# Performance work log

Measured on AMD Instinct MI355X. Metric: run time of the kernel, lower is better.

Reference implementation:

```python
import jax, jax.numpy as jnp
import numpy as np

EPS = 2e-5
NCG = 51  # int(64 / 1.25)

def _conv1d(x, w, d):
    # x: [B,C,L], w: [Co,Ci,K]; dilated 1D conv, SAME padding
    return jax.lax.conv_general_dilated(x, w, window_strides=(1,), padding='SAME',
                                        rhs_dilation=(d,), dimension_numbers=('NCH', 'OIH', 'NCH'))

def _lift(x, w, n_h=9):
    # GConvRdG: lift R1 -> R1xR+; scale h=2^s realized as kernel dilation, 1/h normalization
    return jnp.stack([_conv1d(x, w, 2 ** s) / (2.0 ** s) for s in range(n_h)], axis=2)

def _gg(x, w):
    # GConvGG on [B,C,H,L]; w: [Co,Ci,Nk,K]; h_crop: H_out = H - Nk + 1.
    # Output scale s mixes input scales s..s+Nk-1, each with spatial dilation 2^(s+i).
    Nk, H = w.shape[2], x.shape[2]
    outs = []
    for s in range(H - Nk + 1):
        acc = None
        for i in range(Nk):
            d = 2 ** (s + i)
            t = _conv1d(x[:, :, s + i, :], w[:, :, i, :], d) / float(d)
            acc = t if acc is None else acc + t
        outs.append(acc)
    return jnp.stack(outs, axis=2)

def _bn(x, g, b):
    # training-mode BatchNorm2d over [B,C,H,L], per-channel stats
    m = jnp.mean(x, axis=(0, 2, 3), keepdims=True)
    v = jnp.var(x, axis=(0, 2, 3), keepdims=True)
    return (x - m) * jax.lax.rsqrt(v + EPS) * g[None, :, None, None] + b[None, :, None, None]

def _pool4(x):
    # max_pooling_R1: kernel 4 stride 4 over spatial axis
    B, C, H, L = x.shape
    return jnp.max(x.reshape(B, C, H, L // 4, 4), axis=-1)

def _forward(x, w1, w2, w3, w4, w5, w6, w7, w8, w9, w10, w11,
             g1, b1, g2, b2, g3, b3, g4, b4, g5, b5, g6, b6, g7, b7, g8, b8, g9, b9, g10, b10):
    r = jax.nn.relu
    out = _lift(x, w1)                      # [B,51,9,L]
    out = _pool4(out)
    out = r(_bn(out, g1, b1))
    out = _pool4(out)
    out = r(_bn(_gg(out, w2), g2, b2))      # H 9->7
    out = r(_bn(_gg(out, w3), g3, b3))
    out = _pool4(out)
    out = r(_bn(_gg(out, w4), g4, b4))      # 7->5
    out = r(_bn(_gg(out, w5), g5, b5))
    out = _pool4(out)
    out = r(_bn(_gg(out, w6), g6, b6))      # 5->3
    out = r(_bn(_gg(out, w7), g7, b7))
    out = r(_bn(_gg(out, w8), g8, b8))
    out = _pool4(out)
    out = r(_bn(_gg(out, w9), g9, b9))      # 3->1
    out = r(_bn(_gg(out, w10), g10, b10))
    out = jnp.mean(out, axis=-1, keepdims=True)   # global mean over space -> [B,408,1,1]
    out = _gg(out, w11)                     # 1x1 classifier -> [B,10,1,1]
    out = jnp.max(out, axis=-2)             # max over h axis -> [B,10,1]
    return out.reshape(out.shape[0], 10)

def setup_inputs():
    key = jax.random.key(0)
    ks = jax.random.split(key, 16)
    c = NCG
    def w(k, shape):
        fan_in = float(np.prod(shape[1:]))
        return jax.random.normal(k, shape, jnp.float32) * fan_in ** -0.5
    inp = {
        'x': jax.random.normal(ks[0], (8, 1, 32768), jnp.float32),
        'w1': w(ks[1], (c, 1, 79)),
        'w2': w(ks[2], (c, c, 3, 3)),
        'w3': w(ks[3], (c, c, 1, 3)),
        'w4': w(ks[4], (2 * c, c, 3, 3)),
        'w5': w(ks[5], (2 * c, 2 * c, 1, 3)),
        'w6': w(ks[6], (4 * c, 2 * c, 3, 3)),
        'w7': w(ks[7], (4 * c, 4 * c, 1, 3)),
        'w8': w(ks[8], (4 * c, 4 * c, 1, 3)),
        'w9': w(ks[9], (8 * c, 4 * c, 3, 3)),
        'w10': w(ks[10], (8 * c, 8 * c, 1, 3)),
        'w11': w(ks[11], (10, 8 * c, 1, 1)),
    }
    widths = [c, c, c, 2 * c, 2 * c, 4 * c, 4 * c, 4 * c, 8 * c, 8 * c]
    for i, cw in enumerate(widths, 1):
        inp['g%d' % i] = jnp.ones((cw,), jnp.float32)
        inp['b%d' % i] = jnp.zeros((cw,), jnp.float32)
    return inp

def reference(x, w1, w2, w3, w4, w5, w6, w7, w8, w9, w10, w11,
              g1, b1, g2, b2, g3, b3, g4, b4, g5, b5, g6, b6, g7, b7, g8, b8, g9, b9, g10, b10):
    return _forward(x, w1, w2, w3, w4, w5, w6, w7, w8, w9, w10, w11,
                    g1, b1, g2, b2, g3, b3, g4, b4, g5, b5, g6, b6, g7, b7, g8, b8, g9, b9, g10, b10)
```

## Files before the change

### kernel.cpp

```cpp
#include <hip/hip_runtime.h>
#include <hip/hip_bf16.h>

#define EPSBN 2e-5f

typedef __attribute__((ext_vector_type(8))) short short8v;
typedef __attribute__((ext_vector_type(4))) float f32x4;

__device__ inline unsigned short f2bf(float f) {
  unsigned u = __float_as_uint(f);
  unsigned r = (u + 0x7FFFu + ((u >> 16) & 1u)) >> 16;
  return (unsigned short)r;
}
__device__ inline float bf2f(unsigned short h) {
  return __uint_as_float(((unsigned)h) << 16);
}

template <int CTRL>
__device__ inline float dpp_radd(float v) {
  int r = __builtin_amdgcn_update_dpp(0, __float_as_int(v), CTRL, 0xf, 0xf,
                                      true);
  return v + __int_as_float(r);
}

constexpr int XPADL = 9984;
constexpr int XPADR = 14336;
constexpr int PROW = XPADL + 32768 + XPADR;

__global__ __launch_bounds__(256) void pad_pair_kernel(
    const float* __restrict__ x, unsigned* __restrict__ xpH,
    unsigned* __restrict__ xpL) {
  const int i = blockIdx.x * 256 + threadIdx.x;
  if (i >= PROW) return;
  const int sb = blockIdx.y;
  const int s = sb >> 3;
  const int b = sb & 7;
  const int d = 1 << s;
  const int pos0 = i - XPADL;
  const int pos1 = pos0 + d;
  float v0 = (pos0 >= 0 && pos0 < 32768) ? x[b * 32768 + pos0] : 0.f;
  float v1 = (pos1 >= 0 && pos1 < 32768) ? x[b * 32768 + pos1] : 0.f;
  unsigned u0 = __float_as_uint(v0);
  unsigned h0 = u0 >> 16;
  unsigned lo0 =
      __float_as_uint(v0 - __uint_as_float(u0 & 0xffff0000u)) >> 16;
  unsigned u1 = __float_as_uint(v1);
  unsigned h1 = u1 >> 16;
  unsigned lo1 =
      __float_as_uint(v1 - __uint_as_float(u1 & 0xffff0000u)) >> 16;
  size_t o = (size_t)sb * PROW + i;
  xpH[o] = h0 | (h1 << 16);
  xpL[o] = lo0 | (lo1 << 16);
}

__global__ __launch_bounds__(256) void pack_w1_kernel(
    const float* __restrict__ W, short* __restrict__ A) {
  int idx = blockIdx.x * 256 + threadIdx.x;
  if (idx >= 9 * 64 * 96) return;
  int s = idx / (64 * 96);
  int rem = idx - s * 64 * 96;
  int co = rem / 96;
  int k = rem - co * 96;
  float v = 0.f;
  if (co < 51 && k < 79)
    v = W[co * 79 + k] * __uint_as_float((unsigned)(127 - s) << 23);
  unsigned short hi = f2bf(v);
  unsigned short lo = f2bf(v - bf2f(hi));
  A[(size_t)s * 2 * 64 * 96 + co * 96 + k] = (short)hi;
  A[(size_t)s * 2 * 64 * 96 + 64 * 96 + co * 96 + k] = (short)lo;
}

__global__ __launch_bounds__(256) void lift_mfma_kernel(
    const unsigned* __restrict__ xpH, const unsigned* __restrict__ xpL,
    const short* __restrict__ Apk1, float* __restrict__ y1,
    float* __restrict__ part1) {
  constexpr int P = 104;
  const int bid = blockIdx.x;
  const int lc = (bid & 7) * 64 + (bid >> 3);
  const int s = blockIdx.y;
  const int b = blockIdx.z;
  const int d = 1 << s;
  const int l0 = lc * 64;
  const int tid = threadIdx.x;
  const int lane = tid & 63;
  const int quad = lane >> 4;
  const int n0 = lane & 15;
  const int wv = tid >> 6;
  const int coBase = wv * 16;

  __shared__ __align__(16) short Bh[64 * P];
  __shared__ __align__(16) short Bl[64 * P];
  float* sC = (float*)Bh;

  const int nB = tid & 63;
  const int rowW = ((nB & 3) << 4) | (nB >> 2);
  const int swzW = (nB & 3) << 3;
  const int ogu = __builtin_amdgcn_readfirstlane(tid >> 6);
  const unsigned* xqH = xpH + (size_t)(s * 8 + b) * PROW + XPADL + l0;
  const unsigned* xqL = xpL + (size_t)(s * 8 + b) * PROW + XPADL + l0;

#pragma unroll
  for (int r = 0; r < 3; ++r) {
    const int kb = (ogu + 4 * r) * 8;
    const int base = (kb - 39) * d;
    uint4 ph, pl;
    ph.x = xqH[base + nB];
    ph.y = xqH[base + 2 * d + nB];
    ph.z = xqH[base + 4 * d + nB];
    ph.w = xqH[base + 6 * d + nB];
    pl.x = xqL[base + nB];
    pl.y = xqL[base + 2 * d + nB];
    pl.z = xqL[base + 4 * d + nB];
    pl.w = xqL[base + 6 * d + nB];
    *(uint4*)(Bh + rowW * P + (kb ^ swzW)) = ph;
    *(uint4*)(Bl + rowW * P + (kb ^ swzW)) = pl;
  }

  const short* ApkS = Apk1 + (size_t)s * 2 * 64 * 96;
  const short* arowH = ApkS + (coBase + n0) * 96;
  const short* arowL = arowH + 64 * 96;

  __syncthreads();

  f32x4 acc[4];
#pragma unroll
  for (int t = 0; t < 4; ++t) acc[t] = (f32x4){0.f, 0.f, 0.f, 0.f};

#pragma unroll
  for (int ks = 0; ks < 3; ++ks) {
    short8v ah = *(const short8v*)(arowH + ks * 32 + quad * 8);
    short8v al = *(const short8v*)(arowL + ks * 32 + quad * 8);
#pragma unroll
    for (int t = 0; t < 4; ++t) {
      const int n = n0 + 16 * t;
      const int off = (ks * 32 + quad * 8) ^ (t << 3);
      short8v bh = *(const short8v*)(Bh + n * P + off);
      short8v bl = *(const short8v*)(Bl + n * P + off);
      acc[t] = __builtin_amdgcn_mfma_f32_16x16x32_bf16(ah, bh, acc[t], 0, 0, 0);
      acc[t] = __builtin_amdgcn_mfma_f32_16x16x32_bf16(ah, bl, acc[t], 0, 0, 0);
      acc[t] = __builtin_amdgcn_mfma_f32_16x16x32_bf16(al, bh, acc[t], 0, 0, 0);
    }
  }

  __syncthreads();

#pragma unroll
  for (int reg = 0; reg < 4; ++reg) {
    const int co = coBase + quad * 4 + reg;
    float po = fmaxf(fmaxf(acc[0][reg], acc[1][reg]),
                     fmaxf(acc[2][reg], acc[3][reg]));
    const bool valid = (co < 51);
    if (valid) {
      y1[(((size_t)b * 51 + co) * 9 + s) * 8192 + (l0 >> 2) + n0] = po;
    }
    float us = valid ? po : 0.f;
    float sq = us * us;
    us = dpp_radd<0x128>(us);
    sq = dpp_radd<0x128>(sq);
    us = dpp_radd<0x124>(us);
    sq = dpp_radd<0x124>(sq);
    us = dpp_radd<0x122>(us);
    sq = dpp_radd<0x122>(sq);
    us = dpp_radd<0x121>(us);
    sq = dpp_radd<0x121>(sq);
    if (n0 == 0) {
      sC[co] = us;
      sC[64 + co] = sq;
    }
  }
  __syncthreads();
  if (tid < 51) {
    float* pp = part1 + (size_t)lc * 128;
    atomicAdd(&pp[tid], sC[tid]);
    atomicAdd(&pp[64 + tid], sC[64 + tid]);
  }
}

__global__ __launch_bounds__(128) void reduce_stats1_kernel(
    const float* __restrict__ p, float* __restrict__ st) {
  const int t = threadIdx.x;
  if (t >= 102) return;
  const int k0 = blockIdx.x * 64;
  const int off = (t < 51) ? t : (64 + t - 51);
  float s = 0.f;
  for (int k = k0; k < k0 + 64; ++k) s += p[k * 128 + off];
  atomicAdd(&st[(t < 51) ? t : (512 + t - 51)], s);
}

__global__ __launch_bounds__(256) void stats_kernel(
    const float* __restrict__ Y, float* __restrict__ st, int C, int HL,
    int NS) {
  const int c = blockIdx.x, b = blockIdx.y, z = blockIdx.z;
  const int slice = HL / NS;
  const float* p = Y + ((size_t)b * C + c) * HL + (size_t)z * slice;
  float s = 0.f, q = 0.f;
  for (int i = threadIdx.x; i < slice; i += 256) {
    float v = p[i];
    s += v;
    q += v * v;
  }
#pragma unroll
  for (int off = 32; off > 0; off >>= 1) {
    s += __shfl_down(s, off, 64);
    q += __shfl_down(q, off, 64);
  }
  __shared__ float ls[4], lq[4];
  const int wid = threadIdx.x >> 6, lane = threadIdx.x & 63;
  if (lane == 0) { ls[wid] = s; lq[wid] = q; }
  __syncthreads();
  if (threadIdx.x == 0) {
    atomicAdd(&st[c], ls[0] + ls[1] + ls[2] + ls[3]);
    atomicAdd(&st[512 + c], lq[0] + lq[1] + lq[2] + lq[3]);
  }
}

__global__ __launch_bounds__(256) void reduce_parts_kernel(
    const float* __restrict__ p, float* __restrict__ y, int n, int stride,
    int ns) {
  int i = blockIdx.x * 256 + threadIdx.x;
  if (i >= n) return;
  float s = 0.f;
  for (int k = 0; k < ns; ++k) s += p[(size_t)k * stride + i];
  y[i] = s;
}

__device__ inline void parts_bn(const float* __restrict__ pp, unsigned c,
                                float invN, const float* __restrict__ g,
                                const float* __restrict__ bb, float& sc,
                                float& bi) {
  float ssum = 0.f, sqs = 0.f;
#pragma unroll
  for (int k = 0; k < 8; ++k) {
    ssum += pp[k * 1024 + c];
    sqs += pp[k * 1024 + 512 + c];
  }
  float m = ssum * invN;
  float v = sqs * invN - m * m;
  sc = g[c] * rsqrtf(v + EPSBN);
  bi = bb[c] - m * sc;
}

__global__ __launch_bounds__(256) void bnrelu_pool_parts_kernel(
    const float* __restrict__ Y, const float* __restrict__ pp,
    const float* __restrict__ g, const float* __restrict__ bb,
    float* __restrict__ Z, int C, int H, int Lin, float invN,
    unsigned int total) {
  unsigned int idx = blockIdx.x * 256u + threadIdx.x;
  if (idx >= total) return;
  const unsigned int Lo = (unsigned int)(Lin >> 2);
  unsigned int lo = idx % Lo;
  unsigned int r1 = idx / Lo;
  unsigned int h = r1 % (unsigned int)H;
  unsigned int r2 = r1 / (unsigned int)H;
  unsigned int c = r2 % (unsigned int)C;
  unsigned int b = r2 / (unsigned int)C;
  float sc, bi;
  parts_bn(pp, c, invN, g, bb, sc, bi);
  const float* p = Y + (((size_t)b * C + c) * H + h) * Lin + 4u * lo;
  float a0 = p[0] * sc + bi, a1 = p[1] * sc + bi;
  float a2 = p[2] * sc + bi, a3 = p[3] * sc + bi;
  float r = fmaxf(fmaxf(a0, a1), fmaxf(a2, a3));
  Z[idx] = fmaxf(r, 0.f);
}

__global__ __launch_bounds__(256) void bnrelu_pool_bf16_parts_kernel(
    const float* __restrict__ Y, const float* __restrict__ pp,
    const float* __restrict__ g, const float* __restrict__ bb,
    unsigned short* __restrict__ Z, int C, int H, int Lin, float invN,
    unsigned int total) {
  unsigned int idx = blockIdx.x * 256u + threadIdx.x;
  if (idx >= total) return;
  const unsigned int Lo = (unsigned int)(Lin >> 2);
  unsigned int lo = idx % Lo;
  unsigned int r1 = idx / Lo;
  unsigned int h = r1 % (unsigned int)H;
  unsigned int r2 = r1 / (unsigned int)H;
  unsigned int c = r2 % (unsigned int)C;
  unsigned int b = r2 / (unsigned int)C;
  float sc, bi;
  parts_bn(pp, c, invN, g, bb, sc, bi);
  const float* p = Y + (((size_t)b * C + c) * H + h) * Lin + 4u * lo;
  float a0 = p[0] * sc + bi, a1 = p[1] * sc + bi;
  float a2 = p[2] * sc + bi, a3 = p[3] * sc + bi;
  float r = fmaxf(fmaxf(a0, a1), fmaxf(a2, a3));
  Z[idx] = f2bf(fmaxf(r, 0.f));
}

__global__ __launch_bounds__(256) void bnrelu_pool_bf16_kernel(
    const float* __restrict__ Y, const float* __restrict__ st,
    const float* __restrict__ g, const float* __restrict__ bb,
    unsigned short* __restrict__ Z, int C, int H, int Lin, float invN,
    unsigned int total) {
  unsigned int idx = blockIdx.x * 256u + threadIdx.x;
  if (idx >= total) return;
  const unsigned int Lo = (unsigned int)(Lin >> 2);
  unsigned int lo = idx % Lo;
  unsigned int r1 = idx / Lo;
  unsigned int h = r1 % (unsigned int)H;
  unsigned int r2 = r1 / (unsigned int)H;
  unsigned int c = r2 % (unsigned int)C;
  unsigned int b = r2 / (unsigned int)C;
  float m = st[c] * invN;
  float v = st[512 + c] * invN - m * m;
  float sc = g[c] * rsqrtf(v + EPSBN);
  float bi = bb[c] - m * sc;
  const float* p = Y + (((size_t)b * C + c) * H + h) * Lin + 4u * lo;
  float a0 = p[0] * sc + bi, a1 = p[1] * sc + bi;
  float a2 = p[2] * sc + bi, a3 = p[3] * sc + bi;
  float r = fmaxf(fmaxf(a0, a1), fmaxf(a2, a3));
  Z[idx] = f2bf(fmaxf(r, 0.f));
}

__global__ __launch_bounds__(256) void bnrelu_kernel(
    const float* __restrict__ Y, const float* __restrict__ st,
    const float* __restrict__ g, const float* __restrict__ bb,
    float* __restrict__ A, int C, int HL, float invN, unsigned int total) {
  unsigned int idx = blockIdx.x * 256u + threadIdx.x;
  if (idx >= total) return;
  unsigned int c = (idx / (unsigned int)HL) % (unsigned int)C;
  float m = st[c] * invN;
  float v = st[512 + c] * invN - m * m;
  float sc = g[c] * rsqrtf(v + EPSBN);
  float bi = bb[c] - m * sc;
  A[idx] = fmaxf(fmaf(Y[idx], sc, bi), 0.f);
}

__global__ __launch_bounds__(256) void bnrelu_bf16_parts_kernel(
    const float* __restrict__ Y, const float* __restrict__ pp,
    const float* __restrict__ g, const float* __restrict__ bb,
    unsigned short* __restrict__ A, int C, int HL, float invN,
    unsigned int total) {
  unsigned int idx = blockIdx.x * 256u + threadIdx.x;
  if (idx >= total) return;
  unsigned int c = (idx / (unsigned int)HL) % (unsigned int)C;
  float sc, bi;
  parts_bn(pp, c, invN, g, bb, sc, bi);
  A[idx] = f2bf(fmaxf(fmaf(Y[idx], sc, bi), 0.f));
}

__global__ __launch_bounds__(256) void pack_w2_kernel(
    const float* __restrict__ W, short* __restrict__ A, int Co, int KTOT,
    int KPAD, int COPAD, int NS, int nk3) {
  int idx = blockIdx.x * 256 + threadIdx.x;
  const int CK = COPAD * KPAD;
  if (idx >= NS * CK) return;
  int s = idx / CK;
  int rem = idx - s * CK;
  int co = rem / KPAD;
  int kk = rem - co * KPAD;
  float v = 0.f;
  if (co < Co && kk < KTOT) {
    int i = (kk % nk3) / 3;
    float scale = __uint_as_float((unsigned)(127 - (s + i)) << 23);
    v = W[co * KTOT + kk] * scale;
  }
  unsigned short hi = f2bf(v);
  unsigned short lo = f2bf(v - bf2f(hi));
  A[(size_t)s * 2 * CK + co * KPAD + kk] = (short)hi;
  A[(size_t)s * 2 * CK + CK + co * KPAD + kk] = (short)lo;
}

template <int NKv, int LT>
__global__ __launch_bounds__(256) void gg_mfma5_kernel(
    const unsigned short* __restrict__ X, const short* __restrict__ Apk,
    float* __restrict__ Y, float* __restrict__ part, int Ci, int Co, int Hin,
    int L, int nL, int KTOT, int KPAD, int COPAD) {
  constexpr int T = LT / 16;
  constexpr int KO = 256 / LT;
  constexpr int RIT = 8 / KO;

  const int bx = blockIdx.x;
  const int lc = bx % nL;
  const int cog = bx / nL;
  const int s = blockIdx.y;
  const int b = blockIdx.z;
  const int Hout = Hin - NKv + 1;
  const int l0 = lc * LT;
  const int tid = threadIdx.x;
  const int lane = tid & 63;
  const int quad = lane >> 4;
  const int m0 = lane & 15;
  const int wv = tid >> 6;
  const int coBase = cog * 64 + wv * 16;

  __shared__ __align__(16) short Bh[LT * 72];
  __shared__ int roT[1024];
  __shared__ int shT[1024];
  __shared__ float sCh[2][64];

  for (int kk = tid; kk < KPAD; kk += 256) {
    int ro = 0, sh = -(1 << 30);
    if (kk < KTOT) {
      int ci = kk / (3 * NKv);
      int rem = kk - ci * (3 * NKv);
      int i = rem / 3;
      int k = rem - 3 * i;
      ro = (ci * Hin + s + i) * L;
      sh = (k - 1) * (1 << (s + i));
    }
    roT[kk] = ro;
    shT[kk] = sh;
  }
  __syncthreads();

  f32x4 acc[T];
#pragma unroll
  for (int t = 0; t < T; ++t) acc[t] = (f32x4){0.f, 0.f, 0.f, 0.f};

  const short* ApkS = Apk + (size_t)s * 2 * COPAD * KPAD;
  const short* arowH = ApkS + (size_t)(coBase + m0) * KPAD;
  const short* arowL = arowH + (size_t)COPAD * KPAD;
  const unsigned short* Xb = X + (size_t)b * Ci * Hin * L;

  const int lB = tid & (LT - 1);
  const int oc0 = tid / LT;
  const int nch = (KTOT + 63) >> 6;

  uint4 v0[RIT], v1[RIT], v2[RIT];
  auto gather = [&](int c0, uint4 (&pk)[RIT]) {
#pragma unroll
    for (int r = 0; r < RIT; ++r) {
      const int oct = oc0 + KO * r;
      const int kkb = (c0 << 6) + oct * 8;
      unsigned w[8];
#pragma unroll
      for (int j = 0; j < 8; ++j) {
        const int kk = kkb + j;
        const int pos = l0 + lB + shT[kk];
        const int posc = min(max(pos, 0), L - 1);
        unsigned u = (unsigned)Xb[roT[kk] + posc];
        w[j] = ((unsigned)pos < (unsigned)L) ? u : 0u;
      }
      pk[r].x = w[0] | (w[1] << 16);
      pk[r].y = w[2] | (w[3] << 16);
      pk[r].z = w[4] | (w[5] << 16);
      pk[r].w = w[6] | (w[7] << 16);
    }
  };

  gather(0, v0);
  if (nch > 1) gather(1, v1);
  for (int c0 = 0; c0 < nch; ++c0) {
#pragma unroll
    for (int r = 0; r < RIT; ++r)
      *(uint4*)(Bh + lB * 72 + (oc0 + KO * r) * 8) = v0[r];
    if (c0 + 2 < nch) gather(c0 + 2, v2);
    const int a0 = (c0 << 6) + quad * 8;
    short8v ah0 = *(const short8v*)(arowH + a0);
    short8v al0 = *(const short8v*)(arowL + a0);
    short8v ah1 = *(const short8v*)(arowH + a0 + 32);
    short8v al1 = *(const short8v*)(arowL + a0 + 32);
    __syncthreads();
#pragma unroll
    for (int t = 0; t < T; ++t) {
      const int l = m0 + 16 * t;
      short8v b0 = *(const short8v*)(Bh + l * 72 + quad * 8);
      short8v b1 = *(const short8v*)(Bh + l * 72 + 32 + quad * 8);
      acc[t] = __builtin_amdgcn_mfma_f32_16x16x32_bf16(ah0, b0, acc[t], 0, 0, 0);
      acc[t] = __builtin_amdgcn_mfma_f32_16x16x32_bf16(al0, b0, acc[t], 0, 0, 0);
      acc[t] = __builtin_amdgcn_mfma_f32_16x16x32_bf16(ah1, b1, acc[t], 0, 0, 0);
      acc[t] = __builtin_amdgcn_mfma_f32_16x16x32_bf16(al1, b1, acc[t], 0, 0, 0);
    }
    __syncthreads();
#pragma unroll
    for (int r = 0; r < RIT; ++r) {
      v0[r] = v1[r];
      v1[r] = v2[r];
    }
  }

#pragma unroll
  for (int reg = 0; reg < 4; ++reg) {
    const int co = coBase + quad * 4 + reg;
    float ss = 0.f, sq = 0.f;
    if (co < Co) {
      float* yp = Y + (((size_t)b * Co + co) * Hout + s) * L + l0;
#pragma unroll
      for (int t = 0; t < T; ++t) {
        float v = acc[t][reg];
        yp[m0 + 16 * t] = v;
        ss += v;
        sq = fmaf(v, v, sq);
      }
    }
    ss = dpp_radd<0x128>(ss);
    sq = dpp_radd<0x128>(sq);
    ss = dpp_radd<0x124>(ss);
    sq = dpp_radd<0x124>(sq);
    ss = dpp_radd<0x122>(ss);
    sq = dpp_radd<0x122>(sq);
    ss = dpp_radd<0x121>(ss);
    sq = dpp_radd<0x121>(sq);
    if (m0 == 0) {
      sCh[0][wv * 16 + quad * 4 + reg] = ss;
      sCh[1][wv * 16 + quad * 4 + reg] = sq;
    }
  }
  __syncthreads();
  if (tid < 64) {
    const int co = cog * 64 + tid;
    if (co < Co) {
      float* pp = part + (size_t)(lc & 7) * 1024;
      atomicAdd(&pp[co], sCh[0][tid]);
      atomicAdd(&pp[512 + co], sCh[1][tid]);
    }
  }
}

template <int NK, int L, int COSUB, int UN>
__global__ __launch_bounds__(256) void gg_tail3_kernel(
    const float* __restrict__ X, const float* __restrict__ W,
    float* __restrict__ Y, int Ci, int Co, int Hin, int NSPLIT, int ciPer,
    int partStride) {
  const int l = threadIdx.x % L;
  const int cs = threadIdx.x / L;
  const int co = blockIdx.x * COSUB + cs;
  const int s = blockIdx.y / NSPLIT;
  const int seg = blockIdx.y % NSPLIT;
  const int b = blockIdx.z;
  const int Hout = Hin - NK + 1;
  const int ciBeg = seg * ciPer;
  const int ciEnd = min(Ci, ciBeg + ciPer);

  float acc[NK];
#pragma unroll
  for (int i = 0; i < NK; ++i) acc[i] = 0.f;

  const float* wbase = W + (size_t)co * Ci * NK * 3;
  const float* xbase = X + ((size_t)b * Ci * Hin + s) * L;

  int ci = ciBeg;
  for (; ci + UN <= ciEnd; ci += UN) {
    float xv[UN][NK][3];
#pragma unroll
    for (int u = 0; u < UN; ++u) {
      const float* xr = xbase + (size_t)(ci + u) * (Hin * L);
#pragma unroll
      for (int i = 0; i < NK; ++i) {
        const int d = 1 << (s + i);
        const float* row = xr + i * L;
        xv[u][i][0] = (l >= d) ? row[l - d] : 0.f;
        xv[u][i][1] = row[l];
        xv[u][i][2] = (l + d < L) ? row[l + d] : 0.f;
      }
    }
#pragma unroll
    for (int u = 0; u < UN; ++u) {
      const float* wp = wbase + (ci + u) * (NK * 3);
#pragma unroll
      for (int i = 0; i < NK; ++i)
        acc[i] = fmaf(wp[3 * i], xv[u][i][0],
                      fmaf(wp[3 * i + 1], xv[u][i][1],
                           fmaf(wp[3 * i + 2], xv[u][i][2], acc[i])));
    }
  }
  for (; ci < ciEnd; ++ci) {
    const float* xr = xbase + (size_t)ci * (Hin * L);
    const float* wp = wbase + ci * (NK * 3);
#pragma unroll
    for (int i = 0; i < NK; ++i) {
      const int d = 1 << (s + i);
      const float* row = xr + i * L;
      float xm = (l >= d) ? row[l - d] : 0.f;
      float xc = row[l];
      float xp = (l + d < L) ? row[l + d] : 0.f;
      acc[i] = fmaf(wp[3 * i], xm,
                    fmaf(wp[3 * i + 1], xc, fmaf(wp[3 * i + 2], xp, acc[i])));
    }
  }
  float out = 0.f;
#pragma unroll
  for (int i = 0; i < NK; ++i) {
    float invd = __uint_as_float((unsigned)(127 - (s + i)) << 23);
    out = fmaf(acc[i], invd, out);
  }
  Y[(size_t)seg * partStride + (((size_t)b * Co + co) * Hout + s) * L + l] =
      out;
}

__global__ __launch_bounds__(256) void final_kernel(
    const float* __restrict__ Y, const float* __restrict__ st,
    const float* __restrict__ g, const float* __restrict__ bb,
    const float* __restrict__ w11, float* __restrict__ out) {
  const int b = blockIdx.x;
  const int tid = threadIdx.x;
  __shared__ float tch[408];
  for (int c = tid; c < 408; c += 256) {
    float m = st[c] * (1.f / 256.f);
    float v = st[512 + c] * (1.f / 256.f) - m * m;
    float sc = g[c] * rsqrtf(v + EPSBN);
    float bi = bb[c] - m * sc;
    const float* p = Y + ((size_t)b * 408 + c) * 32;
    float ssum = 0.f;
#pragma unroll
    for (int l = 0; l < 32; ++l) ssum += fmaxf(p[l] * sc + bi, 0.f);
    tch[c] = ssum * (1.f / 32.f);
  }
  __syncthreads();
  if (tid < 10) {
    float ssum = 0.f;
    for (int c = 0; c < 408; ++c) ssum += w11[tid * 408 + c] * tch[c];
    out[b * 10 + tid] = ssum;
  }
}

extern "C" void kernel_launch(void* const* d_in, const int* in_sizes, int n_in,
                              void* d_out, int out_size, void* d_ws,
                              size_t ws_size, hipStream_t stream) {
  const float* x = (const float*)d_in[0];
  const float* w1 = (const float*)d_in[1];
  const float* w2 = (const float*)d_in[2];
  const float* w3 = (const float*)d_in[3];
  const float* w4 = (const float*)d_in[4];
  const float* w5 = (const float*)d_in[5];
  const float* w6 = (const float*)d_in[6];
  const float* w7 = (const float*)d_in[7];
  const float* w8 = (const float*)d_in[8];
  const float* w9 = (const float*)d_in[9];
  const float* w10 = (const float*)d_in[10];
  const float* w11 = (const float*)d_in[11];
  const float* gg[11];
  const float* bbv[11];
  for (int i = 1; i <= 10; ++i) {
    gg[i] = (const float*)d_in[12 + 2 * (i - 1)];
    bbv[i] = (const float*)d_in[12 + 2 * (i - 1) + 1];
  }

  float* ws = (float*)d_ws;
  const size_t AR0 = 0;
  const size_t AR1 = 30081024;
  const size_t STATS = 38900000;
  float* y1 = ws + AR0;
  short* apk1 = (short*)(ws + AR1 + 460800);
  unsigned* xpairH = (unsigned*)(ws + AR1 + 520000);
  unsigned* xpairL = (unsigned*)(ws + AR1 + 4630336);
  float* part1 = ws + AR1 + 8740672;
  unsigned short* z1b = (unsigned short*)(ws + AR1);
  unsigned short* a3b = (unsigned short*)(ws + AR1);
  unsigned short* z3b = (unsigned short*)(ws + AR1);
  unsigned short* a5b = (unsigned short*)(ws + AR1 + 1500000);
  unsigned short* z5b = (unsigned short*)(ws + AR1);
  unsigned short* a6b = (unsigned short*)(ws + AR1 + 522240);
  unsigned short* a7b = (unsigned short*)(ws + AR1 + 1148928);
  float* z8 = ws + AR1;
  float* a9 = ws + AR1 + 1775616;
  float* part9 = ws + AR1 + 1900000;
  float* part10 = ws + AR1 + 2400000;
  float* y2 = ws + AR0;
  float* y3 = ws + AR0 + 5849088;
  float* y4 = ws + AR0;
  float* y5 = ws + AR0 + 2088960;
  float* y6 = ws + AR0;
  float* y7 = ws + AR0 + 626688;
  float* y8 = ws + AR0 + 1253376;
  float* y9 = ws + AR0;
  float* y10 = ws + AR0 + 104448;
  short* apk2 = (short*)(ws + 12000000);
  short* apk3 = apk2 + 7 * 2 * 64 * 512;
  short* apk4 = apk3 + 7 * 2 * 64 * 192;
  short* apk5 = apk4 + 5 * 2 * 128 * 512;
  short* apk6 = apk5 + 5 * 2 * 128 * 320;
  short* apk7 = apk6 + 3 * 2 * 256 * 960;
  short* apk8 = apk7 + 3 * 2 * 256 * 640;
  float* st[11];
  for (int i = 1; i <= 10; ++i) st[i] = ws + STATS + (size_t)(i - 1) * 1024;
  float* partg = ws + STATS + 10240;
  float* part2 = partg;
  float* part3 = partg + 8192;
  float* part4 = partg + 2 * 8192;
  float* part5 = partg + 3 * 8192;
  float* part6 = partg + 4 * 8192;
  float* part7 = partg + 5 * 8192;
  float* part8 = partg + 6 * 8192;

  hipMemsetAsync((void*)(ws + STATS), 0, 10 * 1024 * sizeof(float), stream);
  hipMemsetAsync((void*)part1, 0, 512 * 128 * sizeof(float), stream);
  hipMemsetAsync((void*)partg, 0, 7 * 8192 * sizeof(float), stream);

  pad_pair_kernel<<<dim3((PROW + 255) / 256, 72), 256, 0, stream>>>(
      x, xpairH, xpairL);
  pack_w1_kernel<<<(9 * 64 * 96 + 255) / 256, 256, 0, stream>>>(w1, apk1);
  lift_mfma_kernel<<<dim3(512, 9, 8), 256, 0, stream>>>(xpairH, xpairL, apk1,
                                                        y1, part1);
  reduce_stats1_kernel<<<8, 128, 0, stream>>>(part1, st[1]);
  {
    unsigned int tot = 8u * 51 * 9 * 2048;
    bnrelu_pool_bf16_kernel<<<(tot + 255) / 256, 256, 0, stream>>>(
        y1, st[1], gg[1], bbv[1], z1b, 51, 9, 8192, 1.f / 589824.f, tot);
  }
  pack_w2_kernel<<<(7 * 64 * 512 + 255) / 256, 256, 0, stream>>>(
      w2, apk2, 51, 459, 512, 64, 7, 9);
  pack_w2_kernel<<<(7 * 64 * 192 + 255) / 256, 256, 0, stream>>>(
      w3, apk3, 51, 153, 192, 64, 7, 3);
  pack_w2_kernel<<<(5 * 128 * 512 + 255) / 256, 256, 0, stream>>>(
      w4, apk4, 102, 459, 512, 128, 5, 9);
  pack_w2_kernel<<<(5 * 128 * 320 + 255) / 256, 256, 0, stream>>>(
      w5, apk5, 102, 306, 320, 128, 5, 3);
  pack_w2_kernel<<<(3 * 256 * 960 + 255) / 256, 256, 0, stream>>>(
      w6, apk6, 204, 918, 960, 256, 3, 9);
  pack_w2_kernel<<<(3 * 256 * 640 + 255) / 256, 256, 0, stream>>>(
      w7, apk7, 204, 612, 640, 256, 3, 3);
  pack_w2_kernel<<<(3 * 256 * 640 + 255) / 256, 256, 0, stream>>>(
      w8, apk8, 204, 612, 640, 256, 3, 3);
  gg_mfma5_kernel<3, 64><<<dim3(32, 7, 8), 256, 0, stream>>>(
      z1b, apk2, y2, part2, 51, 51, 9, 2048, 32, 459, 512, 64);
  {
    unsigned int tot = 8u * 51 * 7 * 2048;
    bnrelu_bf16_parts_kernel<<<(tot + 255) / 256, 256, 0, stream>>>(
        y2, part2, gg[2], bbv[2], a3b, 51, 7 * 2048, 1.f / 114688.f, tot);
  }
  gg_mfma5_kernel<1, 64><<<dim3(32, 7, 8), 256, 0, stream>>>(
      a3b, apk3, y3, part3, 51, 51, 7, 2048, 32, 153, 192, 64);
  {
    unsigned int tot = 8u * 51 * 7 * 512;
    bnrelu_pool_bf16_parts_kernel<<<(tot + 255) / 256, 256, 0, stream>>>(
        y3, part3, gg[3], bbv[3], z3b, 51, 7, 2048, 1.f / 114688.f, tot);
  }
  gg_mfma5_kernel<3, 32><<<dim3(32, 5, 8), 256, 0, stream>>>(
      z3b, apk4, y4, part4, 51, 102, 7, 512, 16, 459, 512, 128);
  {
    unsigned int tot = 8u * 102 * 5 * 512;
    bnrelu_bf16_parts_kernel<<<(tot + 255) / 256, 256, 0, stream>>>(
        y4, part4, gg[4], bbv[4], a5b, 102, 5 * 512, 1.f / 20480.f, tot);
  }
  gg_mfma5_kernel<1, 32><<<dim3(32, 5, 8), 256, 0, stream>>>(
      a5b, apk5, y5, part5, 102, 102, 5, 512, 16, 306, 320, 128);
  {
    unsigned int tot = 8u * 102 * 5 * 128;
    bnrelu_pool_bf16_parts_kernel<<<(tot + 255) / 256, 256, 0, stream>>>(
        y5, part5, gg[5], bbv[5], z5b, 102, 5, 512, 1.f / 20480.f, tot);
  }
  gg_mfma5_kernel<3, 32><<<dim3(16, 3, 8), 256, 0, stream>>>(
      z5b, apk6, y6, part6, 102, 204, 5, 128, 4, 918, 960, 256);
  {
    unsigned int tot = 8u * 204 * 3 * 128;
    bnrelu_bf16_parts_kernel<<<(tot + 255) / 256, 256, 0, stream>>>(
        y6, part6, gg[6], bbv[6], a6b, 204, 3 * 128, 1.f / 3072.f, tot);
  }
  gg_mfma5_kernel<1, 32><<<dim3(16, 3, 8), 256, 0, stream>>>(
      a6b, apk7, y7, part7, 204, 204, 3, 128, 4, 612, 640, 256);
  {
    unsigned int tot = 8u * 204 * 3 * 128;
    bnrelu_bf16_parts_kernel<<<(tot + 255) / 256, 256, 0, stream>>>(
        y7, part7, gg[7], bbv[7], a7b, 204, 3 * 128, 1.f / 3072.f, tot);
  }
  gg_mfma5_kernel<1, 32><<<dim3(16, 3, 8), 256, 0, stream>>>(
      a7b, apk8, y8, part8, 204, 204, 3, 128, 4, 612, 640, 256);
  {
    unsigned int tot = 8u * 204 * 3 * 32;
    bnrelu_pool_parts_kernel<<<(tot + 255) / 256, 256, 0, stream>>>(
        y8, part8, gg[8], bbv[8], z8, 204, 3, 128, 1.f / 3072.f, tot);
  }
  gg_tail3_kernel<3, 32, 8, 2><<<dim3(51, 4, 8), 256, 0, stream>>>(
      z8, w9, part9, 204, 408, 3, 4, 51, 104448);
  reduce_parts_kernel<<<(104448 + 255) / 256, 256, 0, stream>>>(
      part9, y9, 104448, 104448, 4);
  stats_kernel<<<dim3(408, 8, 1), 256, 0, stream>>>(y9, st[9], 408, 32, 1);
  {
    unsigned int tot = 8u * 408 * 32;
    bnrelu_kernel<<<(tot + 255) / 256, 256, 0, stream>>>(
        y9, st[9], gg[9], bbv[9], a9, 408, 32, 1.f / 256.f, tot);
  }
  gg_tail3_kernel<1, 32, 8, 8><<<dim3(51, 4, 8), 256, 0, stream>>>(
      a9, w10, part10, 408, 408, 1, 4, 102, 104448);
  reduce_parts_kernel<<<(104448 + 255) / 256, 256, 0, stream>>>(
      part10, y10, 104448, 104448, 4);
  stats_kernel<<<dim3(408, 8, 1), 256, 0, stream>>>(y10, st[10], 408, 32, 1);
  final_kernel<<<dim3(8), 256, 0, stream>>>(y10, st[10], gg[10], bbv[10], w11,
                                            (float*)d_out);
}
```

Baseline: 606.2 us.

## Pad pooled activations with zero halos, merge weight packing, drop a barrier

```diff
diff --git a/kernel.cpp b/kernel.cpp
--- a/kernel.cpp
+++ b/kernel.cpp
@@ -89,7 +89,7 @@
 
   __shared__ __align__(16) short Bh[64 * P];
   __shared__ __align__(16) short Bl[64 * P];
-  float* sC = (float*)Bh;
+  __shared__ float sCh[2][64];
 
   const int nB = tid & 63;
   const int rowW = ((nB & 3) << 4) | (nB >> 2);
@@ -141,8 +141,6 @@
     }
   }
 
-  __syncthreads();
-
 #pragma unroll
   for (int reg = 0; reg < 4; ++reg) {
     const int co = coBase + quad * 4 + reg;
@@ -163,15 +161,15 @@
     us = dpp_radd<0x121>(us);
     sq = dpp_radd<0x121>(sq);
     if (n0 == 0) {
-      sC[co] = us;
-      sC[64 + co] = sq;
+      sCh[0][co] = us;
+      sCh[1][co] = sq;
     }
   }
   __syncthreads();
   if (tid < 51) {
     float* pp = part1 + (size_t)lc * 128;
-    atomicAdd(&pp[tid], sC[tid]);
-    atomicAdd(&pp[64 + tid], sC[64 + tid]);
+    atomicAdd(&pp[tid], sCh[0][tid]);
+    atomicAdd(&pp[64 + tid], sCh[1][tid]);
   }
 }
 
@@ -285,14 +283,22 @@
   Z[idx] = f2bf(fmaxf(r, 0.f));
 }
 
-__global__ __launch_bounds__(256) void bnrelu_pool_bf16_kernel(
+__global__ __launch_bounds__(256) void bnrelu_pool_bf16_pad_kernel(
     const float* __restrict__ Y, const float* __restrict__ st,
     const float* __restrict__ g, const float* __restrict__ bb,
     unsigned short* __restrict__ Z, int C, int H, int Lin, float invN,
-    unsigned int total) {
+    unsigned int total, int Lp, int PADL, unsigned int total2) {
   unsigned int idx = blockIdx.x * 256u + threadIdx.x;
-  if (idx >= total) return;
+  if (idx >= total2) return;
   const unsigned int Lo = (unsigned int)(Lin >> 2);
+  if (idx >= total) {
+    unsigned int hidx = idx - total;
+    unsigned int r = hidx / (unsigned int)(2 * PADL);
+    unsigned int o = hidx - r * (unsigned int)(2 * PADL);
+    unsigned int pos = (o < (unsigned int)PADL) ? o : (Lo + o);
+    Z[(size_t)r * Lp + pos] = 0;
+    return;
+  }
   unsigned int lo = idx % Lo;
   unsigned int r1 = idx / Lo;
   unsigned int h = r1 % (unsigned int)H;
@@ -307,7 +313,38 @@
   float a0 = p[0] * sc + bi, a1 = p[1] * sc + bi;
   float a2 = p[2] * sc + bi, a3 = p[3] * sc + bi;
   float r = fmaxf(fmaxf(a0, a1), fmaxf(a2, a3));
-  Z[idx] = f2bf(fmaxf(r, 0.f));
+  Z[(((size_t)b * C + c) * H + h) * Lp + PADL + lo] = f2bf(fmaxf(r, 0.f));
+}
+
+__global__ __launch_bounds__(256) void bnrelu_pool_bf16_parts_pad_kernel(
+    const float* __restrict__ Y, const float* __restrict__ pp,
+    const float* __restrict__ g, const float* __restrict__ bb,
+    unsigned short* __restrict__ Z, int C, int H, int Lin, float invN,
+    unsigned int total, int Lp, int PADL, unsigned int total2) {
+  unsigned int idx = blockIdx.x * 256u + threadIdx.x;
+  if (idx >= total2) return;
+  const unsigned int Lo = (unsigned int)(Lin >> 2);
+  if (idx >= total) {
+    unsigned int hidx = idx - total;
+    unsigned int r = hidx / (unsigned int)(2 * PADL);
+    unsigned int o = hidx - r * (unsigned int)(2 * PADL);
+    unsigned int pos = (o < (unsigned int)PADL) ? o : (Lo + o);
+    Z[(size_t)r * Lp + pos] = 0;
+    return;
+  }
+  unsigned int lo = idx % Lo;
+  unsigned int r1 = idx / Lo;
+  unsigned int h = r1 % (unsigned int)H;
+  unsigned int r2 = r1 / (unsigned int)H;
+  unsigned int c = r2 % (unsigned int)C;
+  unsigned int b = r2 / (unsigned int)C;
+  float sc, bi;
+  parts_bn(pp, c, invN, g, bb, sc, bi);
+  const float* p = Y + (((size_t)b * C + c) * H + h) * Lin + 4u * lo;
+  float a0 = p[0] * sc + bi, a1 = p[1] * sc + bi;
+  float a2 = p[2] * sc + bi, a3 = p[3] * sc + bi;
+  float r = fmaxf(fmaxf(a0, a1), fmaxf(a2, a3));
+  Z[(((size_t)b * C + c) * H + h) * Lp + PADL + lo] = f2bf(fmaxf(r, 0.f));
 }
 
 __global__ __launch_bounds__(256) void bnrelu_kernel(
@@ -337,14 +374,42 @@
   A[idx] = f2bf(fmaxf(fmaf(Y[idx], sc, bi), 0.f));
 }
 
-__global__ __launch_bounds__(256) void pack_w2_kernel(
-    const float* __restrict__ W, short* __restrict__ A, int Co, int KTOT,
-    int KPAD, int COPAD, int NS, int nk3) {
+__global__ __launch_bounds__(256) void pack_all_kernel(
+    const float* __restrict__ w2, const float* __restrict__ w3,
+    const float* __restrict__ w4, const float* __restrict__ w5,
+    const float* __restrict__ w6, const float* __restrict__ w7,
+    const float* __restrict__ w8, short* __restrict__ apk2) {
   int idx = blockIdx.x * 256 + threadIdx.x;
+  const float* W;
+  short* A;
+  int Co, KTOT, KPAD, COPAD, nk3;
+  int r = idx;
+  if (r < 229376) {
+    W = w2; A = apk2; Co = 51; KTOT = 459; KPAD = 512; COPAD = 64; nk3 = 9;
+  } else if ((r -= 229376) < 86016) {
+    W = w3; A = apk2 + 458752; Co = 51; KTOT = 153; KPAD = 192; COPAD = 64;
+    nk3 = 3;
+  } else if ((r -= 86016) < 327680) {
+    W = w4; A = apk2 + 630784; Co = 102; KTOT = 459; KPAD = 512; COPAD = 128;
+    nk3 = 9;
+  } else if ((r -= 327680) < 204800) {
+    W = w5; A = apk2 + 1286144; Co = 102; KTOT = 306; KPAD = 320; COPAD = 128;
+    nk3 = 3;
+  } else if ((r -= 204800) < 737280) {
+    W = w6; A = apk2 + 1695744; Co = 204; KTOT = 918; KPAD = 960; COPAD = 256;
+    nk3 = 9;
+  } else if ((r -= 737280) < 491520) {
+    W = w7; A = apk2 + 3170304; Co = 204; KTOT = 612; KPAD = 640; COPAD = 256;
+    nk3 = 3;
+  } else if ((r -= 491520) < 491520) {
+    W = w8; A = apk2 + 4153344; Co = 204; KTOT = 612; KPAD = 640; COPAD = 256;
+    nk3 = 3;
+  } else {
+    return;
+  }
   const int CK = COPAD * KPAD;
-  if (idx >= NS * CK) return;
-  int s = idx / CK;
-  int rem = idx - s * CK;
+  int s = r / CK;
+  int rem = r - s * CK;
   int co = rem / KPAD;
   int kk = rem - co * KPAD;
   float v = 0.f;
@@ -359,11 +424,11 @@
   A[(size_t)s * 2 * CK + CK + co * KPAD + kk] = (short)lo;
 }
 
-template <int NKv, int LT>
+template <int NKv, int LT, bool PADDED>
 __global__ __launch_bounds__(256) void gg_mfma5_kernel(
     const unsigned short* __restrict__ X, const short* __restrict__ Apk,
     float* __restrict__ Y, float* __restrict__ part, int Ci, int Co, int Hin,
-    int L, int nL, int KTOT, int KPAD, int COPAD) {
+    int L, int nL, int KTOT, int KPAD, int COPAD, int Lp, int XP) {
   constexpr int T = LT / 16;
   constexpr int KO = 256 / LT;
   constexpr int RIT = 8 / KO;
@@ -388,14 +453,17 @@
   __shared__ float sCh[2][64];
 
   for (int kk = tid; kk < KPAD; kk += 256) {
-    int ro = 0, sh = -(1 << 30);
+    int ro, sh;
     if (kk < KTOT) {
       int ci = kk / (3 * NKv);
       int rem = kk - ci * (3 * NKv);
       int i = rem / 3;
       int k = rem - 3 * i;
-      ro = (ci * Hin + s + i) * L;
+      ro = (ci * Hin + s + i) * Lp + XP;
       sh = (k - 1) * (1 << (s + i));
+    } else {
+      ro = PADDED ? XP : 0;
+      sh = PADDED ? 0 : -(1 << 30);
     }
     roT[kk] = ro;
     shT[kk] = sh;
@@ -409,7 +477,7 @@
   const short* ApkS = Apk + (size_t)s * 2 * COPAD * KPAD;
   const short* arowH = ApkS + (size_t)(coBase + m0) * KPAD;
   const short* arowL = arowH + (size_t)COPAD * KPAD;
-  const unsigned short* Xb = X + (size_t)b * Ci * Hin * L;
+  const unsigned short* Xb = X + (size_t)b * Ci * Hin * Lp;
 
   const int lB = tid & (LT - 1);
   const int oc0 = tid / LT;
@@ -425,10 +493,14 @@
 #pragma unroll
       for (int j = 0; j < 8; ++j) {
         const int kk = kkb + j;
-        const int pos = l0 + lB + shT[kk];
-        const int posc = min(max(pos, 0), L - 1);
-        unsigned u = (unsigned)Xb[roT[kk] + posc];
-        w[j] = ((unsigned)pos < (unsigned)L) ? u : 0u;
+        if (PADDED) {
+          w[j] = (unsigned)Xb[roT[kk] + l0 + lB + shT[kk]];
+        } else {
+          const int pos = l0 + lB + shT[kk];
+          const int posc = min(max(pos, 0), L - 1);
+          unsigned u = (unsigned)Xb[roT[kk] + posc];
+          w[j] = ((unsigned)pos < (unsigned)L) ? u : 0u;
+        }
       }
       pk[r].x = w[0] | (w[1] << 16);
       pk[r].y = w[2] | (w[3] << 16);
@@ -655,12 +727,6 @@
   float* y9 = ws + AR0;
   float* y10 = ws + AR0 + 104448;
   short* apk2 = (short*)(ws + 12000000);
-  short* apk3 = apk2 + 7 * 2 * 64 * 512;
-  short* apk4 = apk3 + 7 * 2 * 64 * 192;
-  short* apk5 = apk4 + 5 * 2 * 128 * 512;
-  short* apk6 = apk5 + 5 * 2 * 128 * 320;
-  short* apk7 = apk6 + 3 * 2 * 256 * 960;
-  short* apk8 = apk7 + 3 * 2 * 256 * 640;
   float* st[11];
   for (int i = 1; i <= 10; ++i) st[i] = ws + STATS + (size_t)(i - 1) * 1024;
   float* partg = ws + STATS + 10240;
@@ -684,67 +750,65 @@
   reduce_stats1_kernel<<<8, 128, 0, stream>>>(part1, st[1]);
   {
     unsigned int tot = 8u * 51 * 9 * 2048;
-    bnrelu_pool_bf16_kernel<<<(tot + 255) / 256, 256, 0, stream>>>(
-        y1, st[1], gg[1], bbv[1], z1b, 51, 9, 8192, 1.f / 589824.f, tot);
-  }
-  pack_w2_kernel<<<(7 * 64 * 512 + 255) / 256, 256, 0, stream>>>(
-      w2, apk2, 51, 459, 512, 64, 7, 9);
-  pack_w2_kernel<<<(7 * 64 * 192 + 255) / 256, 256, 0, stream>>>(
-      w3, apk3, 51, 153, 192, 64, 7, 3);
-  pack_w2_kernel<<<(5 * 128 * 512 + 255) / 256, 256, 0, stream>>>(
-      w4, apk4, 102, 459, 512, 128, 5, 9);
-  pack_w2_kernel<<<(5 * 128 * 320 + 255) / 256, 256, 0, stream>>>(
-      w5, apk5, 102, 306, 320, 128, 5, 3);
-  pack_w2_kernel<<<(3 * 256 * 960 + 255) / 256, 256, 0, stream>>>(
-      w6, apk6, 204, 918, 960, 256, 3, 9);
-  pack_w2_kernel<<<(3 * 256 * 640 + 255) / 256, 256, 0, stream>>>(
-      w7, apk7, 204, 612, 640, 256, 3, 3);
-  pack_w2_kernel<<<(3 * 256 * 640 + 255) / 256, 256, 0, stream>>>(
-      w8, apk8, 204, 612, 640, 256, 3, 3);
-  gg_mfma5_kernel<3, 64><<<dim3(32, 7, 8), 256, 0, stream>>>(
-      z1b, apk2, y2, part2, 51, 51, 9, 2048, 32, 459, 512, 64);
+    unsigned int tot2 = tot + 8u * 51 * 9 * 512;
+    bnrelu_pool_bf16_pad_kernel<<<(tot2 + 255) / 256, 256, 0, stream>>>(
+        y1, st[1], gg[1], bbv[1], z1b, 51, 9, 8192, 1.f / 589824.f, tot, 2560,
+        256, tot2);
+  }
+  pack_all_kernel<<<(2568192 + 255) / 256, 256, 0, stream>>>(
+      w2, w3, w4, w5, w6, w7, w8, apk2);
+  gg_mfma5_kernel<3, 64, true><<<dim3(32, 7, 8), 256, 0, stream>>>(
+      z1b, apk2, y2, part2, 51, 51, 9, 2048, 32, 459, 512, 64, 2560, 256);
   {
     unsigned int tot = 8u * 51 * 7 * 2048;
     bnrelu_bf16_parts_kernel<<<(tot + 255) / 256, 256, 0, stream>>>(
         y2, part2, gg[2], bbv[2], a3b, 51, 7 * 2048, 1.f / 114688.f, tot);
   }
-  gg_mfma5_kernel<1, 64><<<dim3(32, 7, 8), 256, 0, stream>>>(
-      a3b, apk3, y3, part3, 51, 51, 7, 2048, 32, 153, 192, 64);
+  gg_mfma5_kernel<1, 64, false><<<dim3(32, 7, 8), 256, 0, stream>>>(
+      a3b, apk2 + 458752, y3, part3, 51, 51, 7, 2048, 32, 153, 192, 64, 2048,
+      0);
   {
     unsigned int tot = 8u * 51 * 7 * 512;
     bnrelu_pool_bf16_parts_kernel<<<(tot + 255) / 256, 256, 0, stream>>>(
         y3, part3, gg[3], bbv[3], z3b, 51, 7, 2048, 1.f / 114688.f, tot);
   }
-  gg_mfma5_kernel<3, 32><<<dim3(32, 5, 8), 256, 0, stream>>>(
-      z3b, apk4, y4, part4, 51, 102, 7, 512, 16, 459, 512, 128);
+  gg_mfma5_kernel<3, 32, false><<<dim3(32, 5, 8), 256, 0, stream>>>(
+      z3b, apk2 + 630784, y4, part4, 51, 102, 7, 512, 16, 459, 512, 128, 512,
+      0);
   {
     unsigned int tot = 8u * 102 * 5 * 512;
     bnrelu_bf16_parts_kernel<<<(tot + 255) / 256, 256, 0, stream>>>(
         y4, part4, gg[4], bbv[4], a5b, 102, 5 * 512, 1.f / 20480.f, tot);
   }
-  gg_mfma5_kernel<1, 32><<<dim3(32, 5, 8), 256, 0, stream>>>(
-      a5b, apk5, y5, part5, 102, 102, 5, 512, 16, 306, 320, 128);
+  gg_mfma5_kernel<1, 32, false><<<dim3(32, 5, 8), 256, 0, stream>>>(
+      a5b, apk2 + 1286144, y5, part5, 102, 102, 5, 512, 16, 306, 320, 128,
+      512, 0);
   {
     unsigned int tot = 8u * 102 * 5 * 128;
-    bnrelu_pool_bf16_parts_kernel<<<(tot + 255) / 256, 256, 0, stream>>>(
-        y5, part5, gg[5], bbv[5], z5b, 102, 5, 512, 1.f / 20480.f, tot);
-  }
-  gg_mfma5_kernel<3, 32><<<dim3(16, 3, 8), 256, 0, stream>>>(
-      z5b, apk6, y6, part6, 102, 204, 5, 128, 4, 918, 960, 256);
+    unsigned int tot2 = tot + 8u * 102 * 5 * 32;
+    bnrelu_pool_bf16_parts_pad_kernel<<<(tot2 + 255) / 256, 256, 0, stream>>>(
+        y5, part5, gg[5], bbv[5], z5b, 102, 5, 512, 1.f / 20480.f, tot, 160,
+        16, tot2);
+  }
+  gg_mfma5_kernel<3, 32, true><<<dim3(16, 3, 8), 256, 0, stream>>>(
+      z5b, apk2 + 1695744, y6, part6, 102, 204, 5, 128, 4, 918, 960, 256, 160,
+      16);
   {
     unsigned int tot = 8u * 204 * 3 * 128;
     bnrelu_bf16_parts_kernel<<<(tot + 255) / 256, 256, 0, stream>>>(
         y6, part6, gg[6], bbv[6], a6b, 204, 3 * 128, 1.f / 3072.f, tot);
   }
-  gg_mfma5_kernel<1, 32><<<dim3(16, 3, 8), 256, 0, stream>>>(
-      a6b, apk7, y7, part7, 204, 204, 3, 128, 4, 612, 640, 256);
+  gg_mfma5_kernel<1, 32, false><<<dim3(16, 3, 8), 256, 0, stream>>>(
+      a6b, apk2 + 3170304, y7, part7, 204, 204, 3, 128, 4, 612, 640, 256, 128,
+      0);
   {
     unsigned int tot = 8u * 204 * 3 * 128;
     bnrelu_bf16_parts_kernel<<<(tot + 255) / 256, 256, 0, stream>>>(
         y7, part7, gg[7], bbv[7], a7b, 204, 3 * 128, 1.f / 3072.f, tot);
   }
-  gg_mfma5_kernel<1, 32><<<dim3(16, 3, 8), 256, 0, stream>>>(
-      a7b, apk8, y8, part8, 204, 204, 3, 128, 4, 612, 640, 256);
+  gg_mfma5_kernel<1, 32, false><<<dim3(16, 3, 8), 256, 0, stream>>>(
+      a7b, apk2 + 4153344, y8, part8, 204, 204, 3, 128, 4, 612, 640, 256, 128,
+      0);
   {
     unsigned int tot = 8u * 204 * 3 * 32;
     bnrelu_pool_parts_kernel<<<(tot + 255) / 256, 256, 0, stream>>>(
```

Measured after the change: 594.1 us (median of 2 runs). 2.0% less time.
